# Performance work log

Hardware: AMD Instinct MI355X
Metric: run time of the kernel (lower is better)

Reference implementation:

```python
import jax, jax.numpy as jnp
import numpy as np

V = 1000000  # vocab size
NC = 1000    # n_classes
L = 2048     # sentence length
K = 2        # topk


def _conv2d(x, w, b, pad):
    y = jax.lax.conv_general_dilated(
        x, w, window_strides=(1, 1), padding=[(pad, pad), (pad, pad)],
        dimension_numbers=('NCHW', 'OIHW', 'NCHW'))
    return y + b[None, :, None, None]


def _avgpool3s2(x):
    # torch AvgPool2d(kernel=3, stride=2, padding=1), count_include_pad=True -> divide by 9
    s = jax.lax.reduce_window(x, 0.0, jax.lax.add, (1, 1, 3, 3), (1, 1, 2, 2),
                              [(0, 0), (0, 0), (1, 1), (1, 1)])
    return s / 9.0


def setup_inputs() -> dict:
    key = jax.random.key(0)
    ks = jax.random.split(key, 17)
    n = lambda i, shp, sc=0.05: (jax.random.normal(ks[i], shp, jnp.float32) * sc)
    return {
        'image': jax.random.normal(ks[0], (1, 3, 256, 256), jnp.float32),
        'sentence': jax.random.randint(ks[1], (L,), 0, V),
        'conv1_w': n(2, (8, 3, 5, 5)), 'conv1_b': n(3, (8,)),
        'conv2_w': n(4, (8, 8, 5, 5)), 'conv2_b': n(5, (8,)),
        'conv3_w': n(6, (8, 8, 5, 5)), 'conv3_b': n(7, (8,)),
        'emb': n(8, (V, 8)),
        'w_ih': n(9, (24, 8)), 'w_hh': n(10, (24, 8)),
        'b_ih': n(11, (24,)), 'b_hh': n(12, (24,)),
        'conv1x1_w': n(13, (2, 8, 1, 1)), 'conv1x1_b': n(14, (2,)),
        'fc1_w': n(15, (NC, 1024)), 'fc1_b': n(16, (NC,)),
    }


def reference(image, sentence, conv1_w, conv1_b, conv2_w, conv2_b, conv3_w, conv3_b,
              emb, w_ih, w_hh, b_ih, b_hh, conv1x1_w, conv1x1_b, fc1_w, fc1_b):
    # EncoderCNN: relu(pool(conv)) x3, 256 -> 128 -> 64 -> 32
    x = jax.nn.relu(_avgpool3s2(_conv2d(image, conv1_w, conv1_b, 2)))
    x = jax.nn.relu(_avgpool3s2(_conv2d(x, conv2_w, conv2_b, 2)))
    x = jax.nn.relu(_avgpool3s2(_conv2d(x, conv3_w, conv3_b, 2)))  # [1,8,32,32]

    # EncoderRNN: embedding gather + single-layer GRU over the sentence
    emb_seq = emb[sentence]  # [L, 8] memory-bound gather

    def gru_step(h, xt):
        gi = w_ih @ xt + b_ih   # [24]
        gh = w_hh @ h + b_hh    # [24]
        r = jax.nn.sigmoid(gi[:8] + gh[:8])
        z = jax.nn.sigmoid(gi[8:16] + gh[8:16])
        ncand = jnp.tanh(gi[16:] + r * gh[16:])
        return (1.0 - z) * ncand + z * h, None

    h, _ = jax.lax.scan(gru_step, jnp.zeros((8,), x.dtype), emb_seq)  # [8]

    # Fuse: broadcast sentence encoding over 32x32 grid
    encoded_sum = x[0] + h[:, None, None]                 # [8,32,32]
    rep = _conv2d(encoded_sum[None], conv1x1_w, conv1x1_b, 0)[0]  # [2,32,32]

    presence = jnp.sum(rep * rep, axis=0).reshape(-1)     # [1024] L2 presence
    _, topk_idx = jax.lax.top_k(presence, K)
    latent_mask = jnp.zeros_like(presence).at[topk_idx].set(1.0)

    m_vector = jnp.sum(rep, axis=0).reshape(-1)           # [1024]
    attended = m_vector * latent_mask

    logits = attended @ fc1_w.T + fc1_b                   # [NC]
    class_preds = jax.nn.log_softmax(logits[None, :], axis=1)  # [1,NC]
    return class_preds, latent_mask
```

## Files before the change

### kernel.cpp

```cpp
#include <hip/hip_runtime.h>
#include <hip/hip_bf16.h>
#include <math.h>


static __device__ __forceinline__ float bcast_lane(float v, int lane) {
    return __int_as_float(__builtin_amdgcn_readlane(__float_as_int(v), lane));
}
template<int SEL>
static __device__ __forceinline__ float dpp_bcast(float v) {
    return __int_as_float(__builtin_amdgcn_update_dpp(
        0, __float_as_int(v), SEL * 0x55, 0xF, 0xF, true));
}

static __device__ __forceinline__ void release_inc(unsigned* f) {
    __hip_atomic_fetch_add(f, 1u, __ATOMIC_RELEASE, __HIP_MEMORY_SCOPE_AGENT);
}
static __device__ __forceinline__ void spin_until(unsigned* f, unsigned tgt) {
    while (__hip_atomic_load(f, __ATOMIC_ACQUIRE, __HIP_MEMORY_SCOPE_AGENT) < tgt)
        __builtin_amdgcn_s_sleep(2);
}


template<int C_IN, int H_IN>
static __device__ __forceinline__ void conv_pool_relu_item(
    int tid, const float* __restrict__ in, const float* __restrict__ w,
    const float* __restrict__ b, float* __restrict__ out)
{
    const int HO = H_IN / 2;
    if (tid >= 8 * HO * HO) return;
    int ox = tid & (HO - 1);
    int oy = (tid / HO) & (HO - 1);
    int c  = tid / (HO * HO);

    float acc[3][3];
#pragma unroll
    for (int a = 0; a < 3; ++a)
#pragma unroll
        for (int q = 0; q < 3; ++q) acc[a][q] = 0.f;

    const int iy0 = 2 * oy - 3, ix0 = 2 * ox - 3;

    for (int ci = 0; ci < C_IN; ++ci) {
        float tile[7][7];
#pragma unroll
        for (int r = 0; r < 7; ++r) {
            int iy = iy0 + r;
            bool vy = (iy >= 0) && (iy < H_IN);
            const float* rowp = in + ((long long)ci * H_IN + iy) * H_IN;
#pragma unroll
            for (int cc = 0; cc < 7; ++cc) {
                int ix = ix0 + cc;
                bool v = vy && (ix >= 0) && (ix < H_IN);
                tile[r][cc] = v ? rowp[ix] : 0.f;
            }
        }
        const float* wp = w + (c * C_IN + ci) * 25;
        float wk[25];
#pragma unroll
        for (int q = 0; q < 25; ++q) wk[q] = wp[q];
#pragma unroll
        for (int py = 0; py < 3; ++py)
#pragma unroll
            for (int px = 0; px < 3; ++px) {
                float s = acc[py][px];
#pragma unroll
                for (int ky = 0; ky < 5; ++ky)
#pragma unroll
                    for (int kx = 0; kx < 5; ++kx)
                        s = fmaf(tile[py + ky][px + kx], wk[ky * 5 + kx], s);
                acc[py][px] = s;
            }
    }
    float bias = b[c];
    float sum = 0.f;
#pragma unroll
    for (int py = 0; py < 3; ++py) {
        int cy = 2 * oy - 1 + py;
        if (cy < 0 || cy >= H_IN) continue;
#pragma unroll
        for (int px = 0; px < 3; ++px) {
            int cx = 2 * ox - 1 + px;
            if (cx >= 0 && cx < H_IN) sum += acc[py][px] + bias;
        }
    }
    out[tid] = fmaxf(sum * (1.f / 9.f), 0.f);
}

static __device__ __forceinline__ void gi_item(
    int tid, const int* __restrict__ sent, const float* __restrict__ emb,
    const float* __restrict__ w_ih, const float* __restrict__ b_ih,
    const float* __restrict__ b_hh, float* __restrict__ gi)
{
    int t = tid >> 5, L = tid & 31;
    int j = L >> 2, s = L & 3;
    float val;
    if (s == 2) {
        val = b_hh[16 + j];
    } else {
        int row = (s == 0) ? j : (s == 1) ? 8 + j : 16 + j;
        const float* x = emb + (long long)sent[t] * 8;
        const float* wr = w_ih + row * 8;
        float acc = b_ih[row] + (s == 3 ? 0.f : b_hh[row]);
#pragma unroll
        for (int k = 0; k < 8; ++k) acc = fmaf(wr[k], x[k], acc);
        val = acc;
    }
    gi[t * 32 + L] = val;
}

static __device__ __forceinline__ void gru_body(
    const float* __restrict__ gi, const float* __restrict__ w_hh,
    unsigned* flags, float* h_out)
{
    const int L = threadIdx.x & 31;
    const int j = L >> 2, s = L & 3;
    const int row = (s == 0) ? j : (s == 1) ? 8 + j : 16 + j;
    float w[8];
#pragma unroll
    for (int k = 0; k < 8; ++k) w[k] = w_hh[row * 8 + k];

    const float A1 = -1.f / 48.f;
    const float B1 = -1.f / 3.f, B2 = 2.f / 15.f;

    float h0 = 0, h1 = 0, h2 = 0, h3 = 0, h4 = 0, h5 = 0, h6 = 0, h7 = 0;
    float hq = 0.f;

    if (flags) spin_until(&flags[0], 16);

    float pr[8];
#pragma unroll
    for (int i = 0; i < 8; ++i) pr[i] = gi[i * 32 + L];

    const float* gpre = gi + 8 * 32 + L;

    for (int tb = 0; tb < 256; ++tb) {
        if (flags && tb == 15) spin_until(&flags[1], 48);
#pragma unroll
        for (int u = 0; u < 8; ++u) {
            const float g = pr[u];
            pr[u] = gpre[u * 32];

            float a0 = fmaf(w[0], h0, g);
            a0 = fmaf(w[1], h1, a0);
            a0 = fmaf(w[2], h2, a0);
            a0 = fmaf(w[3], h3, a0);
            float a1 = w[4] * h4;
            a1 = fmaf(w[5], h5, a1);
            a1 = fmaf(w[6], h6, a1);
            a1 = fmaf(w[7], h7, a1);
            const float x = a0 + a1;

            const float uux  = x * x;
            const float cx   = A1 * x;
            const float base = fmaf(0.25f, x, 0.5f);
            const float sg   = fmaf(cx, uux, base);

            const float r_b  = dpp_bcast<0>(sg);
            const float z_b  = dpp_bcast<1>(sg);
            const float gn_b = dpp_bcast<3>(g);
            const float y = fmaf(r_b, x, gn_b);

            const float uu = y * y;
            const float v1 = B1 * y;
            const float v2 = B2 * y;
            const float q  = fmaf(v2, uu, v1);
            const float n  = fmaf(q, uu, y);

            const float zh  = z_b * hq;
            const float omz = 1.f - z_b;
            const float n_b = dpp_bcast<2>(n);
            const float hn  = fmaf(omz, n_b, zh);
            hq = hn;
            h0 = bcast_lane(hn, 0);  h1 = bcast_lane(hn, 4);
            h2 = bcast_lane(hn, 8);  h3 = bcast_lane(hn, 12);
            h4 = bcast_lane(hn, 16); h5 = bcast_lane(hn, 20);
            h6 = bcast_lane(hn, 24); h7 = bcast_lane(hn, 28);
        }
        gpre += 256;
    }
    if (threadIdx.x == 0) {
        h_out[0] = h0; h_out[1] = h1; h_out[2] = h2; h_out[3] = h3;
        h_out[4] = h4; h_out[5] = h5; h_out[6] = h6; h_out[7] = h7;
    }
}

static __device__ __forceinline__ void fuse_fc_body256(
    const float* __restrict__ x3, const float* hv8,
    const float* __restrict__ w1, const float* __restrict__ b1,
    const float* __restrict__ W, const float* __restrict__ WT,
    const float* __restrict__ bias,
    float* __restrict__ out)
{
    __shared__ float mvec_s[1024];
    __shared__ float rv[256];
    __shared__ int   ri[256];
    __shared__ float s_red[256];
    __shared__ int   s_i1, s_i2;

    const int tid = threadIdx.x;
    float pres[4];
#pragma unroll
    for (int q = 0; q < 4; ++q) {
        const int i = tid + q * 256;
        float r0 = b1[0], r1 = b1[1];
#pragma unroll
        for (int c = 0; c < 8; ++c) {
            const float e = x3[c * 1024 + i] + hv8[c];
            r0 = fmaf(w1[c], e, r0);
            r1 = fmaf(w1[8 + c], e, r1);
        }
        pres[q] = r0 * r0 + r1 * r1;
        mvec_s[i] = r0 + r1;
    }
    float bv = pres[0]; int bi = tid;
#pragma unroll
    for (int q = 1; q < 4; ++q)
        if (pres[q] > bv) { bv = pres[q]; bi = tid + q * 256; }
    rv[tid] = bv; ri[tid] = bi;
    __syncthreads();
    for (int s = 128; s > 0; s >>= 1) {
        if (tid < s) {
            float ov = rv[tid + s]; int oi = ri[tid + s];
            if (ov > rv[tid] || (ov == rv[tid] && oi < ri[tid])) {
                rv[tid] = ov; ri[tid] = oi;
            }
        }
        __syncthreads();
    }
    if (tid == 0) s_i1 = ri[0];
    __syncthreads();
    const int i1 = s_i1;
    float bv2 = -__builtin_inff(); int bi2 = 1 << 30;
#pragma unroll
    for (int q = 0; q < 4; ++q) {
        const int i = tid + q * 256;
        const float v = (i == i1) ? -__builtin_inff() : pres[q];
        if (v > bv2 || (v == bv2 && i < bi2)) { bv2 = v; bi2 = i; }
    }
    rv[tid] = bv2; ri[tid] = bi2;
    __syncthreads();
    for (int s = 128; s > 0; s >>= 1) {
        if (tid < s) {
            float ov = rv[tid + s]; int oi = ri[tid + s];
            if (ov > rv[tid] || (ov == rv[tid] && oi < ri[tid])) {
                rv[tid] = ov; ri[tid] = oi;
            }
        }
        __syncthreads();
    }
    if (tid == 0) s_i2 = ri[0];
    __syncthreads();
    const int i2 = s_i2;
#pragma unroll
    for (int q = 0; q < 4; ++q) {
        const int i = tid + q * 256;
        out[1000 + i] = (i == i1 || i == i2) ? 1.f : 0.f;
    }
    const float a1 = mvec_s[i1], a2 = mvec_s[i2];

    float lg[4];
    if (WT) {
        const float* c1p = WT + (long long)i1 * 1000;
        const float* c2p = WT + (long long)i2 * 1000;
#pragma unroll
        for (int q = 0; q < 4; ++q) {
            const int c = tid + q * 256;
            lg[q] = (c < 1000)
                ? bias[c] + a1 * c1p[c] + a2 * c2p[c]
                : -__builtin_inff();
        }
    } else {
#pragma unroll
        for (int q = 0; q < 4; ++q) {
            const int c = tid + q * 256;
            lg[q] = (c < 1000)
                ? bias[c] + a1 * W[(long long)c * 1024 + i1]
                          + a2 * W[(long long)c * 1024 + i2]
                : -__builtin_inff();
        }
    }
    s_red[tid] = fmaxf(fmaxf(lg[0], lg[1]), fmaxf(lg[2], lg[3]));
    __syncthreads();
    for (int s = 128; s > 0; s >>= 1) {
        if (tid < s) s_red[tid] = fmaxf(s_red[tid], s_red[tid + s]);
        __syncthreads();
    }
    const float m = s_red[0];
    __syncthreads();
    float eloc = 0.f;
#pragma unroll
    for (int q = 0; q < 4; ++q) eloc += __expf(lg[q] - m);
    s_red[tid] = eloc;
    __syncthreads();
    for (int s = 128; s > 0; s >>= 1) {
        if (tid < s) s_red[tid] += s_red[tid + s];
        __syncthreads();
    }
    const float lse = logf(s_red[0]);
#pragma unroll
    for (int q = 0; q < 4; ++q) {
        const int c = tid + q * 256;
        if (c < 1000) out[c] = lg[q] - m - lse;
    }
}

__global__ __launch_bounds__(256) void mega_k(
    const int* __restrict__ sent, const float* __restrict__ emb,
    const float* __restrict__ wih, const float* __restrict__ bih,
    const float* __restrict__ bhh, float* __restrict__ gi,
    const float* __restrict__ img, const float* __restrict__ c1w,
    const float* __restrict__ c1b, float* __restrict__ x1,
    const float* __restrict__ c2w, const float* __restrict__ c2b,
    float* __restrict__ x2,
    const float* __restrict__ c3w, const float* __restrict__ c3b,
    float* __restrict__ x3,
    const float* __restrict__ whh,
    const float* __restrict__ w1, const float* __restrict__ b1,
    const float* __restrict__ fcw, float* __restrict__ fcwT,
    const float* __restrict__ fcb,
    float* __restrict__ out,
    unsigned* __restrict__ flags)
{
    __shared__ float s_hv[8];
    const int bid = blockIdx.x;
    if (bid == 0) {
        if (threadIdx.x < 64) gru_body(gi, whh, flags, s_hv);
        __syncthreads();
        spin_until(&flags[11], 128);
        fuse_fc_body256(x3, s_hv, w1, b1, fcw, fcwT, fcb, out);
    } else if (bid <= 16) {
        gi_item((bid - 1) * 256 + threadIdx.x, sent, emb, wih, bih, bhh, gi);
        __syncthreads();
        if (threadIdx.x == 0) release_inc(&flags[0]);
    } else if (bid <= 64) {
        const int base = 4096 + (bid - 17) * 1280;
#pragma unroll
        for (int it = 0; it < 5; ++it)
            gi_item(base + it * 256 + threadIdx.x, sent, emb, wih, bih, bhh, gi);
        __syncthreads();
        if (threadIdx.x == 0) release_inc(&flags[1]);
    } else {
        const int cb = bid - 65;
#pragma unroll
        for (int it = 0; it < 4; ++it)
            conv_pool_relu_item<3, 256>(cb * 256 + threadIdx.x + it * 32768,
                                        img, c1w, c1b, x1);
        __syncthreads();
        if (threadIdx.x == 0) { release_inc(&flags[8]); spin_until(&flags[8], 128); }
        __syncthreads();
        conv_pool_relu_item<8, 128>(cb * 256 + threadIdx.x, x1, c2w, c2b, x2);
        __syncthreads();
        if (threadIdx.x == 0) { release_inc(&flags[9]); spin_until(&flags[9], 128); }
        __syncthreads();
        conv_pool_relu_item<8, 64>(cb * 256 + threadIdx.x, x2, c3w, c3b, x3);
        if (fcwT) {
            const int i0 = cb * 8;
#pragma unroll
            for (int it = 0; it < 8; ++it) {
                const int i = i0 + it;
#pragma unroll
                for (int q = 0; q < 4; ++q) {
                    const int c = threadIdx.x + q * 256;
                    if (c < 1000)
                        fcwT[(long long)i * 1000 + c] =
                            fcw[(long long)c * 1024 + i];
                }
            }
        }
        __syncthreads();
        if (threadIdx.x == 0) release_inc(&flags[11]);
    }
}

template<int C_IN, int H_IN>
__global__ __launch_bounds__(256) void conv_pool_relu_k(
    const float* __restrict__ in, const float* __restrict__ w,
    const float* __restrict__ b, float* __restrict__ out)
{
    conv_pool_relu_item<C_IN, H_IN>(blockIdx.x * 256 + threadIdx.x, in, w, b, out);
}

__global__ __launch_bounds__(256) void gi_k(
    const int* __restrict__ sent, const float* __restrict__ emb,
    const float* __restrict__ w_ih, const float* __restrict__ b_ih,
    const float* __restrict__ b_hh, float* __restrict__ gi)
{
    gi_item(blockIdx.x * 256 + threadIdx.x, sent, emb, w_ih, b_ih, b_hh, gi);
}

__global__ __launch_bounds__(64) void gru_k(
    const float* __restrict__ gi, const float* __restrict__ w_hh,
    float* __restrict__ h_out)
{
    gru_body(gi, w_hh, nullptr, h_out);
}

__global__ __launch_bounds__(256) void fuse_fc_k256(
    const float* __restrict__ x3, const float* __restrict__ hv,
    const float* __restrict__ w1, const float* __restrict__ b1,
    const float* __restrict__ W, const float* __restrict__ bias,
    float* __restrict__ out)
{
    fuse_fc_body256(x3, hv, w1, b1, W, nullptr, bias, out);
}

extern "C" void kernel_launch(void* const* d_in, const int* in_sizes, int n_in,
                              void* d_out, int out_size, void* d_ws, size_t ws_size,
                              hipStream_t stream)
{
    const float* image = (const float*)d_in[0];
    const int*   sent  = (const int*)  d_in[1];
    const float* c1w = (const float*)d_in[2];
    const float* c1b = (const float*)d_in[3];
    const float* c2w = (const float*)d_in[4];
    const float* c2b = (const float*)d_in[5];
    const float* c3w = (const float*)d_in[6];
    const float* c3b = (const float*)d_in[7];
    const float* emb = (const float*)d_in[8];
    const float* wih = (const float*)d_in[9];
    const float* whh = (const float*)d_in[10];
    const float* bih = (const float*)d_in[11];
    const float* bhh = (const float*)d_in[12];
    const float* w1  = (const float*)d_in[13];
    const float* b1  = (const float*)d_in[14];
    const float* fcw = (const float*)d_in[15];
    const float* fcb = (const float*)d_in[16];
    float* out = (float*)d_out;

    char* ws = (char*)d_ws;
    if (ws_size >= 951424) {
        float*    gi    = (float*)(ws);
        float*    x1    = (float*)(ws + 263168);
        float*    x2    = (float*)(ws + 787456);
        float*    x3    = (float*)(ws + 918528);
        unsigned* flags = (unsigned*)(ws + 951360);
        float*    fcwT  = (ws_size >= 5047424) ? (float*)(ws + 951424) : nullptr;
        hipMemsetAsync(ws + 951360, 0, 64, stream);
        mega_k<<<193, 256, 0, stream>>>(sent, emb, wih, bih, bhh, gi,
                                        image, c1w, c1b, x1,
                                        c2w, c2b, x2, c3w, c3b, x3,
                                        whh, w1, b1, fcw, fcwT, fcb,
                                        out, flags);
    } else {
        float* gi = (float*)(ws);
        float* x1 = (float*)(ws);
        float* x2 = (float*)(ws + 262144);
        float* x3 = (float*)(ws + 393216);
        float* hv = (float*)(ws + 425984);
        conv_pool_relu_k<3, 256><<<512, 256, 0, stream>>>(image, c1w, c1b, x1);
        conv_pool_relu_k<8, 128><<<128, 256, 0, stream>>>(x1, c2w, c2b, x2);
        conv_pool_relu_k<8, 64><<<32, 256, 0, stream>>>(x2, c3w, c3b, x3);
        gi_k<<<256, 256, 0, stream>>>(sent, emb, wih, bih, bhh, gi);
        gru_k<<<1, 64, 0, stream>>>(gi, whh, hv);
        fuse_fc_k256<<<1, 256, 0, stream>>>(x3, hv, w1, b1, fcw, fcb, out);
    }
}
```

Measured before the change: 187.3 us.

## Precompute 1x1-conv image projection in conv blocks off the GRU critical path

Splits the 1x1 conv over the encoded sum into an image-only part (w1·x3), computed by four conv blocks once conv3 finishes, and a per-channel bias term (w1·h + b1) folded in by the GRU block. This removes the 8-channel x3 reads and FMAs from the serial tail that follows the GRU. It adds two new flag counters, extra spin-waits and two small workspace buffers, and it shifts the workspace layout, which raises the size required for the mega-kernel path.

New measurement: 188.2 us. Within noise of the previous version (+0.5%).

```diff
diff --git a/kernel.cpp b/kernel.cpp
--- a/kernel.cpp
+++ b/kernel.cpp
@@ -185,7 +185,9 @@
 }
 
 static __device__ __forceinline__ void fuse_fc_body256(
-    const float* __restrict__ x3, const float* hv8,
+    const float* __restrict__ x3,
+    const float* __restrict__ A0v, const float* __restrict__ A1v,
+    const float* hv8,
     const float* __restrict__ w1, const float* __restrict__ b1,
     const float* __restrict__ W, const float* __restrict__ WT,
     const float* __restrict__ bias,
@@ -198,16 +200,28 @@
     __shared__ int   s_i1, s_i2;
 
     const int tid = threadIdx.x;
+    float B0 = b1[0], B1v = b1[1];
+#pragma unroll
+    for (int c = 0; c < 8; ++c) {
+        B0  = fmaf(w1[c],     hv8[c], B0);
+        B1v = fmaf(w1[8 + c], hv8[c], B1v);
+    }
     float pres[4];
 #pragma unroll
     for (int q = 0; q < 4; ++q) {
         const int i = tid + q * 256;
-        float r0 = b1[0], r1 = b1[1];
-#pragma unroll
-        for (int c = 0; c < 8; ++c) {
-            const float e = x3[c * 1024 + i] + hv8[c];
-            r0 = fmaf(w1[c], e, r0);
-            r1 = fmaf(w1[8 + c], e, r1);
+        float r0, r1;
+        if (A0v) {
+            r0 = A0v[i] + B0;
+            r1 = A1v[i] + B1v;
+        } else {
+            r0 = B0; r1 = B1v;
+#pragma unroll
+            for (int c = 0; c < 8; ++c) {
+                const float e = x3[c * 1024 + i];
+                r0 = fmaf(w1[c], e, r0);
+                r1 = fmaf(w1[8 + c], e, r1);
+            }
         }
         pres[q] = r0 * r0 + r1 * r1;
         mvec_s[i] = r0 + r1;
@@ -318,6 +332,7 @@
     const float* __restrict__ w1, const float* __restrict__ b1,
     const float* __restrict__ fcw, float* __restrict__ fcwT,
     const float* __restrict__ fcb,
+    float* __restrict__ A0v, float* __restrict__ A1v,
     float* __restrict__ out,
     unsigned* __restrict__ flags)
 {
@@ -327,7 +342,8 @@
         if (threadIdx.x < 64) gru_body(gi, whh, flags, s_hv);
         __syncthreads();
         spin_until(&flags[11], 128);
-        fuse_fc_body256(x3, s_hv, w1, b1, fcw, fcwT, fcb, out);
+        spin_until(&flags[13], 4);
+        fuse_fc_body256(x3, A0v, A1v, s_hv, w1, b1, fcw, fcwT, fcb, out);
     } else if (bid <= 16) {
         gi_item((bid - 1) * 256 + threadIdx.x, sent, emb, wih, bih, bhh, gi);
         __syncthreads();
@@ -353,6 +369,8 @@
         if (threadIdx.x == 0) { release_inc(&flags[9]); spin_until(&flags[9], 128); }
         __syncthreads();
         conv_pool_relu_item<8, 64>(cb * 256 + threadIdx.x, x2, c3w, c3b, x3);
+        __syncthreads();
+        if (threadIdx.x == 0 && cb < 32) release_inc(&flags[12]);
         if (fcwT) {
             const int i0 = cb * 8;
 #pragma unroll
@@ -367,6 +385,21 @@
                 }
             }
         }
+        if (cb < 4 && A0v) {
+            if (threadIdx.x == 0) spin_until(&flags[12], 32);
+            __syncthreads();
+            const int i = cb * 256 + threadIdx.x;
+            float a0 = 0.f, a1 = 0.f;
+#pragma unroll
+            for (int ch = 0; ch < 8; ++ch) {
+                const float v = x3[ch * 1024 + i];
+                a0 = fmaf(w1[ch],     v, a0);
+                a1 = fmaf(w1[8 + ch], v, a1);
+            }
+            A0v[i] = a0; A1v[i] = a1;
+            __syncthreads();
+            if (threadIdx.x == 0) release_inc(&flags[13]);
+        }
         __syncthreads();
         if (threadIdx.x == 0) release_inc(&flags[11]);
     }
@@ -401,7 +434,7 @@
     const float* __restrict__ W, const float* __restrict__ bias,
     float* __restrict__ out)
 {
-    fuse_fc_body256(x3, hv, w1, b1, W, nullptr, bias, out);
+    fuse_fc_body256(x3, nullptr, nullptr, hv, w1, b1, W, nullptr, bias, out);
 }
 
 extern "C" void kernel_launch(void* const* d_in, const int* in_sizes, int n_in,
@@ -428,19 +461,21 @@
     float* out = (float*)d_out;
 
     char* ws = (char*)d_ws;
-    if (ws_size >= 951424) {
+    if (ws_size >= 959616) {
         float*    gi    = (float*)(ws);
         float*    x1    = (float*)(ws + 263168);
         float*    x2    = (float*)(ws + 787456);
         float*    x3    = (float*)(ws + 918528);
         unsigned* flags = (unsigned*)(ws + 951360);
-        float*    fcwT  = (ws_size >= 5047424) ? (float*)(ws + 951424) : nullptr;
+        float*    A0v   = (float*)(ws + 951424);
+        float*    A1v   = (float*)(ws + 955520);
+        float*    fcwT  = (ws_size >= 5055616) ? (float*)(ws + 959616) : nullptr;
         hipMemsetAsync(ws + 951360, 0, 64, stream);
         mega_k<<<193, 256, 0, stream>>>(sent, emb, wih, bih, bhh, gi,
                                         image, c1w, c1b, x1,
                                         c2w, c2b, x2, c3w, c3b, x3,
                                         whh, w1, b1, fcw, fcwT, fcb,
-                                        out, flags);
+                                        A0v, A1v, out, flags);
     } else {
         float* gi = (float*)(ws);
         float* x1 = (float*)(ws);
```
